# Kernel tuning notes

Measured on AMD Instinct MI355X. Metric: run time of the kernel, lower is better.

The kernel has to match this reference:

```python
import jax, jax.numpy as jnp
import numpy as np

B, N, E, D, O = 2, 50000, 500000, 128, 128


def setup_inputs() -> dict:
    key = jax.random.key(0)
    k1, k2, k3, k4, k5 = jax.random.split(key, 5)
    x = jax.random.normal(k1, (B, N, D), dtype=jnp.float32)
    edge_index = jax.random.randint(k2, (2, E), 0, N, dtype=jnp.int32)
    edge_attr = jax.random.normal(k3, (E, D), dtype=jnp.float32)
    W_msg = jax.random.normal(k4, (3 * D, O), dtype=jnp.float32) * 0.05
    b_msg = jnp.zeros((O,), dtype=jnp.float32)
    W_upd = jax.random.normal(k5, (O, O), dtype=jnp.float32) * 0.05
    b_upd = jnp.zeros((O,), dtype=jnp.float32)
    return {"x": x, "edge_index": edge_index, "edge_attr": edge_attr,
            "W_msg": W_msg, "b_msg": b_msg, "W_upd": W_upd, "b_upd": b_upd}


def reference(x, edge_index, edge_attr, W_msg, b_msg, W_upd, b_upd):
    # x: (B, N, D); edge_index: (2, E); edge_attr: (E, D)
    src, dst = edge_index[0], edge_index[1]
    # per-edge message input: [x_src, x_dst, edge_attr] -> (B, E, 3D)
    msg_in = jnp.concatenate(
        [x[:, src], x[:, dst], jnp.broadcast_to(edge_attr[None], (x.shape[0],) + edge_attr.shape)],
        axis=-1)
    msg = msg_in @ W_msg + b_msg  # (B, E, O)
    # scatter-sum messages into destination nodes, per batch
    agg = jax.vmap(lambda m: jax.ops.segment_sum(m, dst, num_segments=N))(msg)  # (B, N, O)
    counts = jax.ops.segment_sum(jnp.ones((dst.shape[0],), dtype=x.dtype), dst, num_segments=N)
    counts = jnp.maximum(counts, 1.0)  # clamp(min=1)
    messages = agg / counts[None, :, None]
    return messages @ W_upd + b_upd  # (B, N, O)
```

## Files before the change

kernel.cpp:

```cpp
#include <hip/hip_runtime.h>

#define BN 2
#define NN 50000
#define EE 500000
#define DD 128
#define OO 128

typedef float f2v __attribute__((ext_vector_type(2)));
typedef __attribute__((ext_vector_type(8))) __bf16 bf16x8;
typedef __attribute__((ext_vector_type(4))) float f32x4;

__global__ __launch_bounds__(128) void wfuse_k(
    const float* __restrict__ Wm, const float* __restrict__ Wu,
    const float* __restrict__ bm, unsigned short* __restrict__ Wph,
    unsigned short* __restrict__ Wpl, float* __restrict__ bmu) {
    const int o = threadIdx.x;
    const int k = blockIdx.x;
    float s = 0.0f;
    if (k < 3 * DD) {
#pragma unroll 4
        for (int j = 0; j < OO; ++j) s += Wm[k * OO + j] * Wu[j * OO + o];
        const unsigned int u = __float_as_uint(s);
        const unsigned short hi = (unsigned short)(u >> 16);
        const float r = s - __uint_as_float(u & 0xffff0000u);
        const unsigned short lo = (unsigned short)(__float_as_uint(r) >> 16);
        const int kstep = k >> 5;
        const int kr = k & 31;
        const int lane = (kr >> 3) * 16 + (o & 15);
        const int ct = o >> 4;
        const int idx = (((kstep * 8) + ct) * 64 + lane) * 8 + (kr & 7);
        Wph[idx] = hi;
        Wpl[idx] = lo;
    } else {
#pragma unroll 4
        for (int j = 0; j < OO; ++j) s += bm[j] * Wu[j * OO + o];
        bmu[o] = s;
    }
}

__global__ __launch_bounds__(256) void hist_k(const int* __restrict__ ei,
                                              int* __restrict__ hist) {
    int gid = blockIdx.x * 256 + threadIdx.x;
    if (gid >= EE) return;
    atomicAdd(&hist[ei[EE + gid]], 1);
}

__global__ __launch_bounds__(256) void scan1_k(const int* __restrict__ hist,
                                               int* __restrict__ bsum) {
    int i = blockIdx.x * 256 + threadIdx.x;
    int v = (i < NN) ? hist[i] : 0;
#pragma unroll
    for (int off = 32; off > 0; off >>= 1) v += __shfl_down(v, off);
    __shared__ int ws[4];
    if ((threadIdx.x & 63) == 0) ws[threadIdx.x >> 6] = v;
    __syncthreads();
    if (threadIdx.x == 0) bsum[blockIdx.x] = ws[0] + ws[1] + ws[2] + ws[3];
}

__global__ __launch_bounds__(256) void scan2_k(const int* __restrict__ bsum,
                                               int* __restrict__ ebsum,
                                               int* __restrict__ offsets,
                                               int nblk) {
    __shared__ int s[256];
    const int t = threadIdx.x;
    int v = (t < nblk) ? bsum[t] : 0;
    s[t] = v;
    __syncthreads();
    for (int off = 1; off < 256; off <<= 1) {
        int u = (t >= off) ? s[t - off] : 0;
        __syncthreads();
        s[t] += u;
        __syncthreads();
    }
    ebsum[t] = s[t] - v;
    if (t == 0) offsets[NN] = EE;
}

__global__ __launch_bounds__(256) void scan3_k(const int* __restrict__ hist,
                                               const int* __restrict__ ebsum,
                                               int* __restrict__ offsets,
                                               int* __restrict__ cursor) {
    __shared__ int s[256];
    const int t = threadIdx.x;
    const int i = blockIdx.x * 256 + t;
    int v = (i < NN) ? hist[i] : 0;
    s[t] = v;
    __syncthreads();
    for (int off = 1; off < 256; off <<= 1) {
        int u = (t >= off) ? s[t - off] : 0;
        __syncthreads();
        s[t] += u;
        __syncthreads();
    }
    int ex = s[t] - v + ebsum[blockIdx.x];
    if (i < NN) { offsets[i] = ex; cursor[i] = ex; }
}

__global__ __launch_bounds__(256) void fill_k(const int* __restrict__ ei,
                                              int* __restrict__ cursor,
                                              int2* __restrict__ ep) {
    int gid = blockIdx.x * 256 + threadIdx.x;
    if (gid >= EE) return;
    int dst = ei[EE + gid];
    int pos = atomicAdd(&cursor[dst], 1);
    ep[pos] = make_int2(gid, ei[gid]);
}

__global__ __launch_bounds__(256) void agg_k(
    const float* __restrict__ x,
    const float* __restrict__ ea,
    const int* __restrict__ offsets,
    const int2* __restrict__ ep,
    float* __restrict__ S,
    float* __restrict__ T,
    float* __restrict__ cnt)
{
    const int n = (blockIdx.x * 256 + threadIdx.x) >> 6;
    if (n >= NN) return;
    const int lane = threadIdx.x & 63;

    const int beg = offsets[n];
    const int end = offsets[n + 1];

    f2v tA = {0, 0}, s0A = {0, 0}, s1A = {0, 0};

    int j = beg;
    for (; j + 3 < end; j += 4) {
        int2 p0 = ep[j], p1 = ep[j + 1], p2 = ep[j + 2], p3 = ep[j + 3];
        f2v v0 = __builtin_nontemporal_load((const f2v*)(ea + (size_t)p0.x * DD) + lane);
        f2v v1 = __builtin_nontemporal_load((const f2v*)(ea + (size_t)p1.x * DD) + lane);
        f2v v2 = __builtin_nontemporal_load((const f2v*)(ea + (size_t)p2.x * DD) + lane);
        f2v v3 = __builtin_nontemporal_load((const f2v*)(ea + (size_t)p3.x * DD) + lane);
        f2v a0 = ((const f2v*)(x + (size_t)p0.y * DD))[lane];
        f2v a1 = ((const f2v*)(x + (size_t)p1.y * DD))[lane];
        f2v a2 = ((const f2v*)(x + (size_t)p2.y * DD))[lane];
        f2v a3 = ((const f2v*)(x + (size_t)p3.y * DD))[lane];
        f2v b0 = ((const f2v*)(x + ((size_t)NN + p0.y) * DD))[lane];
        f2v b1 = ((const f2v*)(x + ((size_t)NN + p1.y) * DD))[lane];
        f2v b2 = ((const f2v*)(x + ((size_t)NN + p2.y) * DD))[lane];
        f2v b3 = ((const f2v*)(x + ((size_t)NN + p3.y) * DD))[lane];
        tA  += v0 + v1 + v2 + v3;
        s0A += a0 + a1 + a2 + a3;
        s1A += b0 + b1 + b2 + b3;
    }
    for (; j < end; ++j) {
        int2 p = ep[j];
        f2v v = __builtin_nontemporal_load((const f2v*)(ea + (size_t)p.x * DD) + lane);
        f2v a = ((const f2v*)(x + (size_t)p.y * DD))[lane];
        f2v b = ((const f2v*)(x + ((size_t)NN + p.y) * DD))[lane];
        tA += v; s0A += a; s1A += b;
    }

    ((f2v*)(T + (size_t)n * DD))[lane] = tA;
    ((f2v*)(S + (size_t)n * DD))[lane] = s0A;
    ((f2v*)(S + ((size_t)NN + n) * DD))[lane] = s1A;
    if (lane == 0) cnt[n] = (float)(end - beg);
}

__global__ __launch_bounds__(256, 4) void gemm_k(
    const float* __restrict__ S,
    const float* __restrict__ T,
    const float* __restrict__ cnt,
    const float* __restrict__ x,
    const unsigned short* __restrict__ Wph,
    const unsigned short* __restrict__ Wpl,
    const float* __restrict__ bmu,
    const float* __restrict__ bu,
    float* __restrict__ out)
{
    __shared__ unsigned short Ahi[64 * 128];
    __shared__ unsigned short Alo[64 * 128];

    const int tid = threadIdx.x;
    const int R0 = blockIdx.x * 64;
    const int wv = tid >> 6;
    const int l = tid & 63;

    const int srow = tid >> 2;
    const int skq = (tid & 3) * 32;
    const int Rs = R0 + srow;
    const bool sv = Rs < BN * NN;
    const int ns = sv ? (Rs < NN ? Rs : Rs - NN) : 0;
    const int swz = (srow & 7) << 4;
    const float cs = sv ? cnt[ns] : 0.0f;

    f32x4 acc[4][2];
#pragma unroll
    for (int i = 0; i < 4; ++i) {
        acc[i][0] = (f32x4){0.0f, 0.0f, 0.0f, 0.0f};
        acc[i][1] = (f32x4){0.0f, 0.0f, 0.0f, 0.0f};
    }

    for (int seg = 0; seg < 3; ++seg) {
        const float4* p = nullptr;
        if (sv) {
            p = (seg == 0) ? (const float4*)(S + (size_t)Rs * DD + skq)
              : (seg == 1) ? (const float4*)(x + (size_t)Rs * DD + skq)
                           : (const float4*)(T + (size_t)ns * DD + skq);
        }
#pragma unroll
        for (int j = 0; j < 4; ++j) {
            float4 u0 = {0, 0, 0, 0}, u1 = {0, 0, 0, 0};
            if (sv) {
                u0 = p[2 * j];
                u1 = p[2 * j + 1];
                if (seg == 1) {
                    u0.x *= cs; u0.y *= cs; u0.z *= cs; u0.w *= cs;
                    u1.x *= cs; u1.y *= cs; u1.z *= cs; u1.w *= cs;
                }
            }
            const float vv[8] = {u0.x, u0.y, u0.z, u0.w, u1.x, u1.y, u1.z, u1.w};
            unsigned int hw[4], lw[4];
#pragma unroll
            for (int i = 0; i < 4; ++i) {
                const unsigned int b0 = __float_as_uint(vv[2 * i]);
                const unsigned int b1 = __float_as_uint(vv[2 * i + 1]);
                const float r0 = vv[2 * i]     - __uint_as_float(b0 & 0xffff0000u);
                const float r1 = vv[2 * i + 1] - __uint_as_float(b1 & 0xffff0000u);
                hw[i] = (b0 >> 16) | (b1 & 0xffff0000u);
                lw[i] = (__float_as_uint(r0) >> 16) | (__float_as_uint(r1) & 0xffff0000u);
            }
            const int byt = srow * 256 + (((skq + j * 8) * 2) ^ swz);
            *(int4*)((char*)Ahi + byt) = make_int4(hw[0], hw[1], hw[2], hw[3]);
            *(int4*)((char*)Alo + byt) = make_int4(lw[0], lw[1], lw[2], lw[3]);
        }
        __syncthreads();

#pragma unroll
        for (int ks = 0; ks < 4; ++ks) {
            bf16x8 ah[4], al[4];
#pragma unroll
            for (int rt = 0; rt < 4; ++rt) {
                const int row = rt * 16 + (l & 15);
                const int rb = row * 256 +
                               ((ks * 64 + (l >> 4) * 16) ^ ((row & 7) << 4));
                ah[rt] = *(const bf16x8*)((const char*)Ahi + rb);
                al[rt] = *(const bf16x8*)((const char*)Alo + rb);
            }
            const int kg = seg * 4 + ks;
#pragma unroll
            for (int ct = 0; ct < 2; ++ct) {
                const size_t fi =
                    (size_t)(((kg * 8) + (wv * 2 + ct)) * 64 + l) * 8;
                const bf16x8 wh = *(const bf16x8*)(Wph + fi);
                const bf16x8 wl = *(const bf16x8*)(Wpl + fi);
#pragma unroll
                for (int rt = 0; rt < 4; ++rt) {
                    acc[rt][ct] = __builtin_amdgcn_mfma_f32_16x16x32_bf16(
                        ah[rt], wh, acc[rt][ct], 0, 0, 0);
                    acc[rt][ct] = __builtin_amdgcn_mfma_f32_16x16x32_bf16(
                        al[rt], wh, acc[rt][ct], 0, 0, 0);
                    acc[rt][ct] = __builtin_amdgcn_mfma_f32_16x16x32_bf16(
                        ah[rt], wl, acc[rt][ct], 0, 0, 0);
                }
            }
        }
        __syncthreads();
    }

    const int col0 = wv * 32 + (l & 15);
    const float bm0 = bmu[col0], bm1 = bmu[col0 + 16];
    const float bu0 = bu[col0], bu1 = bu[col0 + 16];
    const int rbase = (l >> 4) * 4;
#pragma unroll
    for (int rt = 0; rt < 4; ++rt) {
#pragma unroll
        for (int r = 0; r < 4; ++r) {
            const int Rr = R0 + rt * 16 + rbase + r;
            if (Rr < BN * NN) {
                const int nr = (Rr < NN) ? Rr : Rr - NN;
                const float c = cnt[nr];
                const float inv = 1.0f / fmaxf(c, 1.0f);
                const float g = (c > 0.0f) ? 1.0f : 0.0f;
                __builtin_nontemporal_store(
                    acc[rt][0][r] * inv + g * bm0 + bu0,
                    out + (size_t)Rr * OO + col0);
                __builtin_nontemporal_store(
                    acc[rt][1][r] * inv + g * bm1 + bu1,
                    out + (size_t)Rr * OO + col0 + 16);
            }
        }
    }
}

extern "C" void kernel_launch(void* const* d_in, const int* in_sizes, int n_in,
                              void* d_out, int out_size, void* d_ws, size_t ws_size,
                              hipStream_t stream) {
    const float* x  = (const float*)d_in[0];
    const int*   ei = (const int*)d_in[1];
    const float* ea = (const float*)d_in[2];
    const float* Wm = (const float*)d_in[3];
    const float* bm = (const float*)d_in[4];
    const float* Wu = (const float*)d_in[5];
    const float* bu = (const float*)d_in[6];
    float* out = (float*)d_out;

    float* S   = (float*)d_ws;
    float* T   = S + (size_t)BN * NN * DD;
    float* cnt = T + (size_t)NN * DD;
    float* bmu = cnt + NN;
    unsigned short* Wph = (unsigned short*)(bmu + OO);
    unsigned short* Wpl = Wph + 3 * DD * OO;
    int* offsets = (int*)(Wpl + 3 * DD * OO);
    int* cursor  = offsets + 50004;
    int* hist    = cursor + NN;
    int* bsum    = hist + NN;
    int* ebsum   = bsum + 256;
    int2* ep     = (int2*)(ebsum + 256);

    const int nscan = (NN + 255) / 256;

    hipMemsetAsync(hist, 0, NN * sizeof(int), stream);

    wfuse_k<<<3 * DD + 1, 128, 0, stream>>>(Wm, Wu, bm, Wph, Wpl, bmu);
    hist_k<<<(EE + 255) / 256, 256, 0, stream>>>(ei, hist);
    scan1_k<<<nscan, 256, 0, stream>>>(hist, bsum);
    scan2_k<<<1, 256, 0, stream>>>(bsum, ebsum, offsets, nscan);
    scan3_k<<<nscan, 256, 0, stream>>>(hist, ebsum, offsets, cursor);
    fill_k<<<(EE + 255) / 256, 256, 0, stream>>>(ei, cursor, ep);

    agg_k<<<(NN + 3) / 4, 256, 0, stream>>>(x, ea, offsets, ep, S, T, cnt);

    const int nblocks = (BN * NN + 63) / 64;
    gemm_k<<<nblocks, 256, 0, stream>>>(S, T, cnt, x, Wph, Wpl, bmu, bu, out);
}
```

Before: 560.9 us.

## Fuse neighbor aggregation into GEMM kernel with degree-sorted node ordering

Merges the gather/aggregation kernel into the GEMM kernel, so that per-node sums of x_src and edge_attr go straight into shared memory as the bf16 hi/lo split. This removes the S/T intermediate buffers and their global write and re-read. Nodes are bucketed by in-degree through a small counting sort (three extra tiny kernels), so that each 32-node block sees similar edge counts and load imbalance drops. Each block covers both batches for 32 nodes and shares the edge_attr sum between them. The cost is much higher register pressure, now with 3 waves per SIMD, and a change from one wavefront per node to 4 threads per row doing the gather.

```diff
diff --git a/kernel.cpp b/kernel.cpp
--- a/kernel.cpp
+++ b/kernel.cpp
@@ -6,9 +6,25 @@
 #define DD 128
 #define OO 128
 
-typedef float f2v __attribute__((ext_vector_type(2)));
 typedef __attribute__((ext_vector_type(8))) __bf16 bf16x8;
 typedef __attribute__((ext_vector_type(4))) float f32x4;
+
+__device__ __forceinline__ void cvt8(const f32x4 a, const f32x4 b,
+                                     int4& hi, int4& lo) {
+    const float v[8] = {a[0], a[1], a[2], a[3], b[0], b[1], b[2], b[3]};
+    unsigned int hw[4], lw[4];
+#pragma unroll
+    for (int i = 0; i < 4; ++i) {
+        const unsigned int b0 = __float_as_uint(v[2 * i]);
+        const unsigned int b1 = __float_as_uint(v[2 * i + 1]);
+        const float r0 = v[2 * i]     - __uint_as_float(b0 & 0xffff0000u);
+        const float r1 = v[2 * i + 1] - __uint_as_float(b1 & 0xffff0000u);
+        hw[i] = (b0 >> 16) | (b1 & 0xffff0000u);
+        lw[i] = (__float_as_uint(r0) >> 16) | (__float_as_uint(r1) & 0xffff0000u);
+    }
+    hi = make_int4(hw[0], hw[1], hw[2], hw[3]);
+    lo = make_int4(lw[0], lw[1], lw[2], lw[3]);
+}
 
 __global__ __launch_bounds__(128) void wfuse_k(
     const float* __restrict__ Wm, const float* __restrict__ Wu,
@@ -106,62 +122,43 @@
     ep[pos] = make_int2(gid, ei[gid]);
 }
 
-__global__ __launch_bounds__(256) void agg_k(
+__global__ __launch_bounds__(256) void dhist_k(const int* __restrict__ hist,
+                                               int* __restrict__ hist2) {
+    int i = blockIdx.x * 256 + threadIdx.x;
+    if (i >= NN) return;
+    int d = hist[i]; d = d > 63 ? 63 : d;
+    atomicAdd(&hist2[63 - d], 1);
+}
+
+__global__ __launch_bounds__(64) void dscan_k(const int* __restrict__ hist2,
+                                              int* __restrict__ cur2) {
+    const int t = threadIdx.x;
+    int v = hist2[t];
+    int s = v;
+#pragma unroll
+    for (int off = 1; off < 64; off <<= 1) {
+        int u = __shfl_up(s, off);
+        if (t >= off) s += u;
+    }
+    cur2[t] = s - v;
+}
+
+__global__ __launch_bounds__(256) void dplace_k(const int* __restrict__ hist,
+                                                int* __restrict__ cur2,
+                                                int* __restrict__ perm) {
+    int i = blockIdx.x * 256 + threadIdx.x;
+    if (i >= NN) return;
+    int d = hist[i]; d = d > 63 ? 63 : d;
+    int pos = atomicAdd(&cur2[63 - d], 1);
+    perm[pos] = i;
+}
+
+__global__ __launch_bounds__(256, 3) void fused_k(
     const float* __restrict__ x,
     const float* __restrict__ ea,
     const int* __restrict__ offsets,
     const int2* __restrict__ ep,
-    float* __restrict__ S,
-    float* __restrict__ T,
-    float* __restrict__ cnt)
-{
-    const int n = (blockIdx.x * 256 + threadIdx.x) >> 6;
-    if (n >= NN) return;
-    const int lane = threadIdx.x & 63;
-
-    const int beg = offsets[n];
-    const int end = offsets[n + 1];
-
-    f2v tA = {0, 0}, s0A = {0, 0}, s1A = {0, 0};
-
-    int j = beg;
-    for (; j + 3 < end; j += 4) {
-        int2 p0 = ep[j], p1 = ep[j + 1], p2 = ep[j + 2], p3 = ep[j + 3];
-        f2v v0 = __builtin_nontemporal_load((const f2v*)(ea + (size_t)p0.x * DD) + lane);
-        f2v v1 = __builtin_nontemporal_load((const f2v*)(ea + (size_t)p1.x * DD) + lane);
-        f2v v2 = __builtin_nontemporal_load((const f2v*)(ea + (size_t)p2.x * DD) + lane);
-        f2v v3 = __builtin_nontemporal_load((const f2v*)(ea + (size_t)p3.x * DD) + lane);
-        f2v a0 = ((const f2v*)(x + (size_t)p0.y * DD))[lane];
-        f2v a1 = ((const f2v*)(x + (size_t)p1.y * DD))[lane];
-        f2v a2 = ((const f2v*)(x + (size_t)p2.y * DD))[lane];
-        f2v a3 = ((const f2v*)(x + (size_t)p3.y * DD))[lane];
-        f2v b0 = ((const f2v*)(x + ((size_t)NN + p0.y) * DD))[lane];
-        f2v b1 = ((const f2v*)(x + ((size_t)NN + p1.y) * DD))[lane];
-        f2v b2 = ((const f2v*)(x + ((size_t)NN + p2.y) * DD))[lane];
-        f2v b3 = ((const f2v*)(x + ((size_t)NN + p3.y) * DD))[lane];
-        tA  += v0 + v1 + v2 + v3;
-        s0A += a0 + a1 + a2 + a3;
-        s1A += b0 + b1 + b2 + b3;
-    }
-    for (; j < end; ++j) {
-        int2 p = ep[j];
-        f2v v = __builtin_nontemporal_load((const f2v*)(ea + (size_t)p.x * DD) + lane);
-        f2v a = ((const f2v*)(x + (size_t)p.y * DD))[lane];
-        f2v b = ((const f2v*)(x + ((size_t)NN + p.y) * DD))[lane];
-        tA += v; s0A += a; s1A += b;
-    }
-
-    ((f2v*)(T + (size_t)n * DD))[lane] = tA;
-    ((f2v*)(S + (size_t)n * DD))[lane] = s0A;
-    ((f2v*)(S + ((size_t)NN + n) * DD))[lane] = s1A;
-    if (lane == 0) cnt[n] = (float)(end - beg);
-}
-
-__global__ __launch_bounds__(256, 4) void gemm_k(
-    const float* __restrict__ S,
-    const float* __restrict__ T,
-    const float* __restrict__ cnt,
-    const float* __restrict__ x,
+    const int* __restrict__ perm,
     const unsigned short* __restrict__ Wph,
     const unsigned short* __restrict__ Wpl,
     const float* __restrict__ bmu,
@@ -170,62 +167,83 @@
 {
     __shared__ unsigned short Ahi[64 * 128];
     __shared__ unsigned short Alo[64 * 128];
+    __shared__ float cntS[32];
+    __shared__ int nidS[32];
 
     const int tid = threadIdx.x;
-    const int R0 = blockIdx.x * 64;
+    const int srow = tid >> 2;
+    const int q = tid & 3;
+    const int b = srow >> 5;
+    const int i = srow & 31;
+    const int idx = blockIdx.x * 32 + i;
+    const bool nv = idx < NN;
+    const int n = nv ? perm[idx] : 0;
+    const int beg = nv ? offsets[n] : 0;
+    const int end = nv ? offsets[n + 1] : 0;
+    if (b == 0 && q == 0) { cntS[i] = (float)(end - beg); nidS[i] = n; }
+
+    const float* xb = x + (size_t)(b ? NN : 0) * DD;
+
+    f32x4 sA[8], tp[4];
+#pragma unroll
+    for (int f = 0; f < 8; ++f) sA[f] = (f32x4){0, 0, 0, 0};
+#pragma unroll
+    for (int f = 0; f < 4; ++f) tp[f] = (f32x4){0, 0, 0, 0};
+
+    int j = beg;
+    for (; j + 1 < end; j += 2) {
+        const int2 p0 = ep[j], p1 = ep[j + 1];
+        const f32x4* x0 = (const f32x4*)(xb + (size_t)p0.y * DD) + q * 8;
+        const f32x4* x1 = (const f32x4*)(xb + (size_t)p1.y * DD) + q * 8;
+        const f32x4* e0 = (const f32x4*)(ea + (size_t)p0.x * DD) + q * 8 + b * 4;
+        const f32x4* e1 = (const f32x4*)(ea + (size_t)p1.x * DD) + q * 8 + b * 4;
+#pragma unroll
+        for (int f = 0; f < 8; ++f) sA[f] += x0[f];
+#pragma unroll
+        for (int f = 0; f < 4; ++f) tp[f] += e0[f];
+#pragma unroll
+        for (int f = 0; f < 8; ++f) sA[f] += x1[f];
+#pragma unroll
+        for (int f = 0; f < 4; ++f) tp[f] += e1[f];
+    }
+    if (j < end) {
+        const int2 p = ep[j];
+        const f32x4* x0 = (const f32x4*)(xb + (size_t)p.y * DD) + q * 8;
+        const f32x4* e0 = (const f32x4*)(ea + (size_t)p.x * DD) + q * 8 + b * 4;
+#pragma unroll
+        for (int f = 0; f < 8; ++f) sA[f] += x0[f];
+#pragma unroll
+        for (int f = 0; f < 4; ++f) tp[f] += e0[f];
+    }
+
+    const f32x4* xs = (const f32x4*)(xb + (size_t)n * DD) + q * 8;
+    f32x4 xv[8];
+#pragma unroll
+    for (int f = 0; f < 8; ++f) xv[f] = xs[f];
+
+    const int rowb = srow * 256;
+    const int swz = (srow & 7) << 4;
+
+#pragma unroll
+    for (int h = 0; h < 4; ++h) {
+        int4 hi, lo;
+        cvt8(sA[2 * h], sA[2 * h + 1], hi, lo);
+        const int byt = rowb + ((q * 64 + h * 16) ^ swz);
+        *(int4*)((char*)Ahi + byt) = hi;
+        *(int4*)((char*)Alo + byt) = lo;
+    }
+
     const int wv = tid >> 6;
     const int l = tid & 63;
 
-    const int srow = tid >> 2;
-    const int skq = (tid & 3) * 32;
-    const int Rs = R0 + srow;
-    const bool sv = Rs < BN * NN;
-    const int ns = sv ? (Rs < NN ? Rs : Rs - NN) : 0;
-    const int swz = (srow & 7) << 4;
-    const float cs = sv ? cnt[ns] : 0.0f;
-
     f32x4 acc[4][2];
 #pragma unroll
-    for (int i = 0; i < 4; ++i) {
-        acc[i][0] = (f32x4){0.0f, 0.0f, 0.0f, 0.0f};
-        acc[i][1] = (f32x4){0.0f, 0.0f, 0.0f, 0.0f};
-    }
-
-    for (int seg = 0; seg < 3; ++seg) {
-        const float4* p = nullptr;
-        if (sv) {
-            p = (seg == 0) ? (const float4*)(S + (size_t)Rs * DD + skq)
-              : (seg == 1) ? (const float4*)(x + (size_t)Rs * DD + skq)
-                           : (const float4*)(T + (size_t)ns * DD + skq);
-        }
-#pragma unroll
-        for (int j = 0; j < 4; ++j) {
-            float4 u0 = {0, 0, 0, 0}, u1 = {0, 0, 0, 0};
-            if (sv) {
-                u0 = p[2 * j];
-                u1 = p[2 * j + 1];
-                if (seg == 1) {
-                    u0.x *= cs; u0.y *= cs; u0.z *= cs; u0.w *= cs;
-                    u1.x *= cs; u1.y *= cs; u1.z *= cs; u1.w *= cs;
-                }
-            }
-            const float vv[8] = {u0.x, u0.y, u0.z, u0.w, u1.x, u1.y, u1.z, u1.w};
-            unsigned int hw[4], lw[4];
-#pragma unroll
-            for (int i = 0; i < 4; ++i) {
-                const unsigned int b0 = __float_as_uint(vv[2 * i]);
-                const unsigned int b1 = __float_as_uint(vv[2 * i + 1]);
-                const float r0 = vv[2 * i]     - __uint_as_float(b0 & 0xffff0000u);
-                const float r1 = vv[2 * i + 1] - __uint_as_float(b1 & 0xffff0000u);
-                hw[i] = (b0 >> 16) | (b1 & 0xffff0000u);
-                lw[i] = (__float_as_uint(r0) >> 16) | (__float_as_uint(r1) & 0xffff0000u);
-            }
-            const int byt = srow * 256 + (((skq + j * 8) * 2) ^ swz);
-            *(int4*)((char*)Ahi + byt) = make_int4(hw[0], hw[1], hw[2], hw[3]);
-            *(int4*)((char*)Alo + byt) = make_int4(lw[0], lw[1], lw[2], lw[3]);
-        }
-        __syncthreads();
-
+    for (int rt = 0; rt < 4; ++rt) {
+        acc[rt][0] = (f32x4){0, 0, 0, 0};
+        acc[rt][1] = (f32x4){0, 0, 0, 0};
+    }
+
+    auto mfma_seg = [&](const int seg) {
 #pragma unroll
         for (int ks = 0; ks < 4; ++ks) {
             bf16x8 ah[4], al[4];
@@ -255,8 +273,45 @@
                 }
             }
         }
-        __syncthreads();
-    }
+    };
+
+    __syncthreads();
+    mfma_seg(0);
+    __syncthreads();
+
+    {
+        const float c = (float)(end - beg);
+#pragma unroll
+        for (int h = 0; h < 4; ++h) {
+            int4 hi, lo;
+            cvt8(xv[2 * h] * c, xv[2 * h + 1] * c, hi, lo);
+            const int byt = rowb + ((q * 64 + h * 16) ^ swz);
+            *(int4*)((char*)Ahi + byt) = hi;
+            *(int4*)((char*)Alo + byt) = lo;
+        }
+    }
+    __syncthreads();
+    mfma_seg(1);
+    __syncthreads();
+
+    {
+        const int colb = q * 64 + b * 32;
+        const int r0 = i * 256;
+        const int r1 = (i + 32) * 256;
+        const int sz = (i & 7) << 4;
+#pragma unroll
+        for (int h = 0; h < 2; ++h) {
+            int4 hi, lo;
+            cvt8(tp[2 * h], tp[2 * h + 1], hi, lo);
+            const int cb = (colb + h * 16) ^ sz;
+            *(int4*)((char*)Ahi + r0 + cb) = hi;
+            *(int4*)((char*)Alo + r0 + cb) = lo;
+            *(int4*)((char*)Ahi + r1 + cb) = hi;
+            *(int4*)((char*)Alo + r1 + cb) = lo;
+        }
+    }
+    __syncthreads();
+    mfma_seg(2);
 
     const int col0 = wv * 32 + (l & 15);
     const float bm0 = bmu[col0], bm1 = bmu[col0 + 16];
@@ -266,18 +321,21 @@
     for (int rt = 0; rt < 4; ++rt) {
 #pragma unroll
         for (int r = 0; r < 4; ++r) {
-            const int Rr = R0 + rt * 16 + rbase + r;
-            if (Rr < BN * NN) {
-                const int nr = (Rr < NN) ? Rr : Rr - NN;
-                const float c = cnt[nr];
-                const float inv = 1.0f / fmaxf(c, 1.0f);
-                const float g = (c > 0.0f) ? 1.0f : 0.0f;
+            const int lr = rt * 16 + rbase + r;
+            const int li = lr & 31;
+            if (blockIdx.x * 32 + li < NN) {
+                const int lb = lr >> 5;
+                const int nn = nidS[li];
+                const float cc = cntS[li];
+                const float inv = 1.0f / fmaxf(cc, 1.0f);
+                const float g = (cc > 0.0f) ? 1.0f : 0.0f;
+                const size_t R = (size_t)(lb ? NN : 0) + nn;
                 __builtin_nontemporal_store(
                     acc[rt][0][r] * inv + g * bm0 + bu0,
-                    out + (size_t)Rr * OO + col0);
+                    out + R * OO + col0);
                 __builtin_nontemporal_store(
                     acc[rt][1][r] * inv + g * bm1 + bu1,
-                    out + (size_t)Rr * OO + col0 + 16);
+                    out + R * OO + col0 + 16);
             }
         }
     }
@@ -295,32 +353,34 @@
     const float* bu = (const float*)d_in[6];
     float* out = (float*)d_out;
 
-    float* S   = (float*)d_ws;
-    float* T   = S + (size_t)BN * NN * DD;
-    float* cnt = T + (size_t)NN * DD;
-    float* bmu = cnt + NN;
-    unsigned short* Wph = (unsigned short*)(bmu + OO);
+    unsigned short* Wph = (unsigned short*)d_ws;
     unsigned short* Wpl = Wph + 3 * DD * OO;
-    int* offsets = (int*)(Wpl + 3 * DD * OO);
+    float* bmu   = (float*)(Wpl + 3 * DD * OO);
+    int* offsets = (int*)(bmu + OO);
     int* cursor  = offsets + 50004;
     int* hist    = cursor + NN;
-    int* bsum    = hist + NN;
+    int* hist2   = hist + NN;
+    int* cur2    = hist2 + 64;
+    int* perm    = cur2 + 64;
+    int* bsum    = perm + NN;
     int* ebsum   = bsum + 256;
     int2* ep     = (int2*)(ebsum + 256);
 
     const int nscan = (NN + 255) / 256;
 
-    hipMemsetAsync(hist, 0, NN * sizeof(int), stream);
+    hipMemsetAsync(hist, 0, (NN + 64) * sizeof(int), stream);
 
     wfuse_k<<<3 * DD + 1, 128, 0, stream>>>(Wm, Wu, bm, Wph, Wpl, bmu);
     hist_k<<<(EE + 255) / 256, 256, 0, stream>>>(ei, hist);
     scan1_k<<<nscan, 256, 0, stream>>>(hist, bsum);
     scan2_k<<<1, 256, 0, stream>>>(bsum, ebsum, offsets, nscan);
     scan3_k<<<nscan, 256, 0, stream>>>(hist, ebsum, offsets, cursor);
+    dhist_k<<<nscan, 256, 0, stream>>>(hist, hist2);
+    dscan_k<<<1, 64, 0, stream>>>(hist2, cur2);
+    dplace_k<<<nscan, 256, 0, stream>>>(hist, cur2, perm);
     fill_k<<<(EE + 255) / 256, 256, 0, stream>>>(ei, cursor, ep);
 
-    agg_k<<<(NN + 3) / 4, 256, 0, stream>>>(x, ea, offsets, ep, S, T, cnt);
-
-    const int nblocks = (BN * NN + 63) / 64;
-    gemm_k<<<nblocks, 256, 0, stream>>>(S, T, cnt, x, Wph, Wpl, bmu, bu, out);
-}
+    const int nblocks = (NN + 31) / 32;
+    fused_k<<<nblocks, 256, 0, stream>>>(x, ea, offsets, ep, perm,
+                                         Wph, Wpl, bmu, bu, out);
+}
```

Result: slower. 893.8 us (+59.3%).

## Merge weight prep with histogram and collapse three-pass scan into one kernel

Applied to the files above, without the earlier changes.

Combines the weight-fusion kernel and the destination histogram into one launch with block-range dispatch, and replaces the three-kernel prefix scan with a single 1024-thread block in which each thread scans 49 entries serially. This cuts the launch count in the CSR-building prologue and drops the intermediate block-sum buffers. The single-block scan leaves most of the GPU idle and uses strided, uncoalesced per-thread reads over the histogram, which could cost more than the launches it saves.

```diff
diff --git a/kernel.cpp b/kernel.cpp
--- a/kernel.cpp
+++ b/kernel.cpp
@@ -10,90 +10,72 @@
 typedef __attribute__((ext_vector_type(8))) __bf16 bf16x8;
 typedef __attribute__((ext_vector_type(4))) float f32x4;
 
-__global__ __launch_bounds__(128) void wfuse_k(
+#define WBLK 193
+__global__ __launch_bounds__(256) void prep_k(
     const float* __restrict__ Wm, const float* __restrict__ Wu,
     const float* __restrict__ bm, unsigned short* __restrict__ Wph,
-    unsigned short* __restrict__ Wpl, float* __restrict__ bmu) {
-    const int o = threadIdx.x;
-    const int k = blockIdx.x;
-    float s = 0.0f;
-    if (k < 3 * DD) {
+    unsigned short* __restrict__ Wpl, float* __restrict__ bmu,
+    const int* __restrict__ ei, int* __restrict__ hist) {
+    if (blockIdx.x < WBLK) {
+        const int k = blockIdx.x * 2 + (threadIdx.x >> 7);
+        const int o = threadIdx.x & 127;
+        if (k > 3 * DD) return;
+        float s = 0.0f;
+        if (k < 3 * DD) {
 #pragma unroll 4
-        for (int j = 0; j < OO; ++j) s += Wm[k * OO + j] * Wu[j * OO + o];
-        const unsigned int u = __float_as_uint(s);
-        const unsigned short hi = (unsigned short)(u >> 16);
-        const float r = s - __uint_as_float(u & 0xffff0000u);
-        const unsigned short lo = (unsigned short)(__float_as_uint(r) >> 16);
-        const int kstep = k >> 5;
-        const int kr = k & 31;
-        const int lane = (kr >> 3) * 16 + (o & 15);
-        const int ct = o >> 4;
-        const int idx = (((kstep * 8) + ct) * 64 + lane) * 8 + (kr & 7);
-        Wph[idx] = hi;
-        Wpl[idx] = lo;
+            for (int j = 0; j < OO; ++j) s += Wm[k * OO + j] * Wu[j * OO + o];
+            const unsigned int u = __float_as_uint(s);
+            const unsigned short hi = (unsigned short)(u >> 16);
+            const float r = s - __uint_as_float(u & 0xffff0000u);
+            const unsigned short lo = (unsigned short)(__float_as_uint(r) >> 16);
+            const int kstep = k >> 5;
+            const int kr = k & 31;
+            const int lane = (kr >> 3) * 16 + (o & 15);
+            const int ct = o >> 4;
+            const int idx = (((kstep * 8) + ct) * 64 + lane) * 8 + (kr & 7);
+            Wph[idx] = hi;
+            Wpl[idx] = lo;
+        } else {
+#pragma unroll 4
+            for (int j = 0; j < OO; ++j) s += bm[j] * Wu[j * OO + o];
+            bmu[o] = s;
+        }
     } else {
-#pragma unroll 4
-        for (int j = 0; j < OO; ++j) s += bm[j] * Wu[j * OO + o];
-        bmu[o] = s;
-    }
-}
-
-__global__ __launch_bounds__(256) void hist_k(const int* __restrict__ ei,
-                                              int* __restrict__ hist) {
-    int gid = blockIdx.x * 256 + threadIdx.x;
-    if (gid >= EE) return;
-    atomicAdd(&hist[ei[EE + gid]], 1);
-}
-
-__global__ __launch_bounds__(256) void scan1_k(const int* __restrict__ hist,
-                                               int* __restrict__ bsum) {
-    int i = blockIdx.x * 256 + threadIdx.x;
-    int v = (i < NN) ? hist[i] : 0;
-#pragma unroll
-    for (int off = 32; off > 0; off >>= 1) v += __shfl_down(v, off);
-    __shared__ int ws[4];
-    if ((threadIdx.x & 63) == 0) ws[threadIdx.x >> 6] = v;
+        const int gid = (blockIdx.x - WBLK) * 256 + threadIdx.x;
+        if (gid >= EE) return;
+        atomicAdd(&hist[ei[EE + gid]], 1);
+    }
+}
+
+__global__ __launch_bounds__(1024) void scan_k(const int* __restrict__ hist,
+                                               int* __restrict__ offsets,
+                                               int* __restrict__ cursor) {
+    __shared__ int s[1024];
+    const int t = threadIdx.x;
+    const int base = t * 49;
+    int tot = 0;
+    for (int u = 0; u < 49; ++u) {
+        const int i = base + u;
+        tot += (i < NN) ? hist[i] : 0;
+    }
+    s[t] = tot;
     __syncthreads();
-    if (threadIdx.x == 0) bsum[blockIdx.x] = ws[0] + ws[1] + ws[2] + ws[3];
-}
-
-__global__ __launch_bounds__(256) void scan2_k(const int* __restrict__ bsum,
-                                               int* __restrict__ ebsum,
-                                               int* __restrict__ offsets,
-                                               int nblk) {
-    __shared__ int s[256];
-    const int t = threadIdx.x;
-    int v = (t < nblk) ? bsum[t] : 0;
-    s[t] = v;
-    __syncthreads();
-    for (int off = 1; off < 256; off <<= 1) {
+    for (int off = 1; off < 1024; off <<= 1) {
         int u = (t >= off) ? s[t - off] : 0;
         __syncthreads();
         s[t] += u;
         __syncthreads();
     }
-    ebsum[t] = s[t] - v;
+    int run = s[t] - tot;
+    for (int u = 0; u < 49; ++u) {
+        const int i = base + u;
+        if (i < NN) {
+            offsets[i] = run;
+            cursor[i] = run;
+            run += hist[i];
+        }
+    }
     if (t == 0) offsets[NN] = EE;
-}
-
-__global__ __launch_bounds__(256) void scan3_k(const int* __restrict__ hist,
-                                               const int* __restrict__ ebsum,
-                                               int* __restrict__ offsets,
-                                               int* __restrict__ cursor) {
-    __shared__ int s[256];
-    const int t = threadIdx.x;
-    const int i = blockIdx.x * 256 + t;
-    int v = (i < NN) ? hist[i] : 0;
-    s[t] = v;
-    __syncthreads();
-    for (int off = 1; off < 256; off <<= 1) {
-        int u = (t >= off) ? s[t - off] : 0;
-        __syncthreads();
-        s[t] += u;
-        __syncthreads();
-    }
-    int ex = s[t] - v + ebsum[blockIdx.x];
-    if (i < NN) { offsets[i] = ex; cursor[i] = ex; }
 }
 
 __global__ __launch_bounds__(256) void fill_k(const int* __restrict__ ei,
@@ -304,20 +286,15 @@
     int* offsets = (int*)(Wpl + 3 * DD * OO);
     int* cursor  = offsets + 50004;
     int* hist    = cursor + NN;
-    int* bsum    = hist + NN;
-    int* ebsum   = bsum + 256;
-    int2* ep     = (int2*)(ebsum + 256);
-
-    const int nscan = (NN + 255) / 256;
+    int2* ep     = (int2*)(hist + NN);
 
     hipMemsetAsync(hist, 0, NN * sizeof(int), stream);
 
-    wfuse_k<<<3 * DD + 1, 128, 0, stream>>>(Wm, Wu, bm, Wph, Wpl, bmu);
-    hist_k<<<(EE + 255) / 256, 256, 0, stream>>>(ei, hist);
-    scan1_k<<<nscan, 256, 0, stream>>>(hist, bsum);
-    scan2_k<<<1, 256, 0, stream>>>(bsum, ebsum, offsets, nscan);
-    scan3_k<<<nscan, 256, 0, stream>>>(hist, ebsum, offsets, cursor);
-    fill_k<<<(EE + 255) / 256, 256, 0, stream>>>(ei, cursor, ep);
+    const int nhist = (EE + 255) / 256;
+    prep_k<<<WBLK + nhist, 256, 0, stream>>>(Wm, Wu, bm, Wph, Wpl, bmu,
+                                             ei, hist);
+    scan_k<<<1, 1024, 0, stream>>>(hist, offsets, cursor);
+    fill_k<<<nhist, 256, 0, stream>>>(ei, cursor, ep);
 
     agg_k<<<(NN + 3) / 4, 256, 0, stream>>>(x, ea, offsets, ep, S, T, cnt);
 
```

After: 665.1 us. +18.6%, slower.
